# Optimization experiments

Hardware: AMD Instinct MI355X
Metric: run time of the kernel (lower is better)

Reference implementation:

```python
import jax, jax.numpy as jnp
import numpy as np

D_MODEL = 1024
N_HEADS = 16
D_K = D_MODEL // N_HEADS
B, T = 2, 2048


def setup_inputs() -> dict:
    key = jax.random.key(0)
    ks = jax.random.split(key, 9)
    s = 1.0 / np.sqrt(D_MODEL)
    def lin(kw, kb):
        W = jax.random.uniform(kw, (D_MODEL, D_MODEL), jnp.float32, -s, s)
        b = jax.random.uniform(kb, (D_MODEL,), jnp.float32, -s, s)
        return W, b
    Wq, bq = lin(ks[0], ks[1])
    Wk, bk = lin(ks[2], ks[3])
    Wv, bv = lin(ks[4], ks[5])
    Wo, bo = lin(ks[6], ks[7])
    x = jax.random.normal(ks[8], (B, T, D_MODEL), jnp.float32)
    return {"x": x, "Wq": Wq, "bq": bq, "Wk": Wk, "bk": bk,
            "Wv": Wv, "bv": bv, "Wo": Wo, "bo": bo}


def reference(x, Wq, bq, Wk, bk, Wv, bv, Wo, bo):
    Bn, Tn, _ = x.shape
    # torch Linear: x @ W.T + b
    def proj(W, b):
        y = x @ W.T + b  # [B, T, D]
        return y.reshape(Bn, Tn, N_HEADS, D_K).transpose(0, 2, 1, 3)  # [B, H, T, d_k]
    q = proj(Wq, bq)
    k = proj(Wk, bk)
    v = proj(Wv, bv)
    scores = jnp.einsum('bhqd,bhkd->bhqk', q, k) / jnp.sqrt(jnp.float32(D_K))
    causal = jnp.tril(jnp.ones((Tn, Tn), dtype=bool))  # True = keep
    scores = jnp.where(causal[None, None], scores, -jnp.inf)
    attn = jax.nn.softmax(scores, axis=-1)
    # dropout is identity in eval mode
    ctx = jnp.einsum('bhqk,bhkd->bhqd', attn, v)
    ctx = ctx.transpose(0, 2, 1, 3).reshape(Bn, Tn, D_MODEL)
    return ctx @ Wo.T + bo
```

## Files before the change

### kernel.cpp

```cpp
#include <hip/hip_runtime.h>
#include <hip/hip_bf16.h>
#include <stdint.h>

#define D_MODEL 1024
#define NH 16
#define DK 64
#define BB 2
#define TT 2048
#define NROWS (BB*TT)

#define QSCALE 0.180336880f

typedef short bf16x8 __attribute__((ext_vector_type(8)));
typedef short bf16x4 __attribute__((ext_vector_type(4)));
typedef float f32x4  __attribute__((ext_vector_type(4)));

#if __has_builtin(__builtin_amdgcn_mfma_f32_16x16x16_bf16)
  #define MFMA16(a,b,c) __builtin_amdgcn_mfma_f32_16x16x16_bf16(a,b,c,0,0,0)
  #define HAVE_M16 1
#elif __has_builtin(__builtin_amdgcn_mfma_f32_16x16x16bf16_1k)
  #define MFMA16(a,b,c) __builtin_amdgcn_mfma_f32_16x16x16bf16_1k(a,b,c,0,0,0)
  #define HAVE_M16 1
#else
  #define HAVE_M16 0
#endif

#if __has_builtin(__builtin_amdgcn_global_load_lds)
  #define HAVE_GLDS 1
__device__ __forceinline__ void gload16(const unsigned short* g, unsigned short* lds){
    __builtin_amdgcn_global_load_lds(
        (const __attribute__((address_space(1))) unsigned int*)g,
        (__attribute__((address_space(3))) unsigned int*)lds, 16, 0, 0);
}
#else
  #define HAVE_GLDS 0
#endif

__device__ __forceinline__ float fexp2(float x){
#if __has_builtin(__builtin_amdgcn_exp2f)
    return __builtin_amdgcn_exp2f(x);
#else
    return exp2f(x);
#endif
}

__device__ __forceinline__ unsigned pkbf(float a, float b){
    float2 t; t.x = a; t.y = b;
    __hip_bfloat162 h = __float22bfloat162_rn(t);
    return *reinterpret_cast<unsigned*>(&h);
}
__device__ __forceinline__ unsigned short bfbits(float a){
    __hip_bfloat16 h = __float2bfloat16(a);
    return *reinterpret_cast<unsigned short*>(&h);
}

__global__ __launch_bounds__(256) void conv_all(
    const float* __restrict__ x,
    const float* __restrict__ Wq, const float* __restrict__ Wk,
    const float* __restrict__ Wv, const float* __restrict__ Wo,
    unsigned short* __restrict__ xb, unsigned short* __restrict__ wb)
{
    const int blk = blockIdx.x;
    const float* src; unsigned short* dst; size_t i;
    if (blk < 2048) {
        src = x; dst = xb;
        i = ((size_t)blk * 256 + threadIdx.x) * 8;
    } else {
        const int t = (blk - 2048) >> 9;
        src = (t == 0) ? Wq : (t == 1) ? Wk : (t == 2) ? Wv : Wo;
        dst = wb + (size_t)t * D_MODEL * D_MODEL;
        i = ((size_t)((blk - 2048) & 511) * 256 + threadIdx.x) * 8;
    }
    float4 a = *(const float4*)(src + i);
    float4 b = *(const float4*)(src + i + 4);
    uint4 w;
    w.x = pkbf(a.x, a.y); w.y = pkbf(a.z, a.w);
    w.z = pkbf(b.x, b.y); w.w = pkbf(b.z, b.w);
    *(uint4*)(dst + i) = w;
}

__global__ __launch_bounds__(256) void conv_bf16(
    const float* __restrict__ x, unsigned short* __restrict__ y)
{
    size_t i = ((size_t)blockIdx.x * 256 + threadIdx.x) * 8;
    float4 a = *(const float4*)(x + i);
    float4 b = *(const float4*)(x + i + 4);
    uint4 w;
    w.x = pkbf(a.x, a.y); w.y = pkbf(a.z, a.w);
    w.z = pkbf(b.x, b.y); w.w = pkbf(b.z, b.w);
    *(uint4*)(y + i) = w;
}

#if HAVE_GLDS
template<int MI, int NB, bool CF32>
__device__ __forceinline__ void gemm_async(
    const unsigned short* __restrict__ Ap, const unsigned short* __restrict__ Bp,
    const float* __restrict__ bias, void* __restrict__ Cp,
    bool vt, float scale, unsigned short* As, unsigned short* Bs)
{
    constexpr int BMt = MI * 32, BNt = NB * 32;
    const int K = D_MODEL, N = D_MODEL;
    const int tid  = threadIdx.x;
    const int m0   = blockIdx.y * BMt;
    const int n0   = blockIdx.x * BNt;
    const int lane = tid & 63;
    const int w    = tid >> 6;
    const int wm   = (w >> 1) * (MI * 16);
    const int wn   = (w &  1) * (BNt / 2);
    const int l16  = lane & 15;
    const int quad = lane >> 4;
    const int crow = lane >> 2;
    const int ccol = (lane & 3) * 8;

    constexpr int CA = MI / 2;
    constexpr int CB = NB / 2;

    auto issue = [&](int buf, int k0){
        #pragma unroll
        for (int c = 0; c < CA; ++c) {
            const int chunk = w * CA + c;
            gload16(Ap + (size_t)(m0 + chunk*16 + crow) * K + k0 + ccol,
                    As + buf * BMt * 32 + chunk * 512);
        }
        #pragma unroll
        for (int c = 0; c < CB; ++c) {
            const int chunk = w * CB + c;
            gload16(Bp + (size_t)(n0 + chunk*16 + crow) * K + k0 + ccol,
                    Bs + buf * BNt * 32 + chunk * 512);
        }
    };

    f32x4 acc[MI][NB] = {};
    issue(0, 0);

    constexpr int ITER = D_MODEL / 32;
    for (int it = 0; it < ITER; ++it) {
        __syncthreads();
        if (it + 1 < ITER) issue((it + 1) & 1, (it + 1) * 32);
        const unsigned short* A = As + (it & 1) * BMt * 32;
        const unsigned short* B = Bs + (it & 1) * BNt * 32;
        bf16x8 af[MI], bg[NB];
        #pragma unroll
        for (int i = 0; i < MI; ++i)
            af[i] = *(const bf16x8*)&A[(wm + 16*i + l16) * 32 + quad * 8];
        #pragma unroll
        for (int j = 0; j < NB; ++j)
            bg[j] = *(const bf16x8*)&B[(wn + 16*j + l16) * 32 + quad * 8];
        #pragma unroll
        for (int i = 0; i < MI; ++i)
            #pragma unroll
            for (int j = 0; j < NB; ++j)
                acc[i][j] = __builtin_amdgcn_mfma_f32_16x16x32_bf16(af[i], bg[j], acc[i][j], 0, 0, 0);
    }

    #pragma unroll
    for (int j = 0; j < NB; ++j) {
        const int n = n0 + wn + 16*j + l16;
        const float bj = bias[n];
        #pragma unroll
        for (int i = 0; i < MI; ++i) {
            const int m = m0 + wm + 16*i + quad*4;
            if (vt) {
                const int b = m >> 11, t = m & 2047;
                ushort4 wv;
                wv.x = bfbits(acc[i][j][0] + bj);
                wv.y = bfbits(acc[i][j][1] + bj);
                wv.z = bfbits(acc[i][j][2] + bj);
                wv.w = bfbits(acc[i][j][3] + bj);
                *(ushort4*)((unsigned short*)Cp + (size_t)b * D_MODEL * TT
                            + (size_t)n * TT + t) = wv;
            } else {
                #pragma unroll
                for (int r = 0; r < 4; ++r) {
                    float v = (acc[i][j][r] + bj) * scale;
                    if (CF32) ((float*)Cp)[(size_t)(m + r) * N + n] = v;
                    else      ((__hip_bfloat16*)Cp)[(size_t)(m + r) * N + n] = __float2bfloat16(v);
                }
            }
        }
    }
}
#endif

#define ASTR 40

template<int MI, int NB, bool AF32, bool BF32, bool CF32>
__device__ __forceinline__ void gemm_body(
    const void* __restrict__ Ap, const void* __restrict__ Bp,
    const float* __restrict__ bias, void* __restrict__ Cp,
    bool vt, float scale, unsigned short* As, unsigned short* Bs)
{
    constexpr int BMt = MI * 32, BNt = NB * 32;
    const int K = D_MODEL, N = D_MODEL;
    const int tid  = threadIdx.x;
    const int m0   = blockIdx.y * BMt;
    const int n0   = blockIdx.x * BNt;
    const int lane = tid & 63;
    const int wave = tid >> 6;
    const int wm   = (wave >> 1) * (MI * 16);
    const int wn   = (wave &  1) * (BNt / 2);
    const int l16  = lane & 15;
    const int quad = lane >> 4;
    const int ar = (MI == 4) ? (tid >> 1) : (tid >> 2);
    const int ac = (MI == 4) ? ((tid & 1) * 16) : ((tid & 3) * 8);
    const int br = (NB == 4) ? (tid >> 1) : (tid >> 2);
    const int bc = (NB == 4) ? ((tid & 1) * 16) : ((tid & 3) * 8);

    uint4 pa[4], pb[4];

    auto loadA = [&](int k0){
        if (AF32) {
            const float* p = (const float*)Ap + (size_t)(m0 + ar) * K + k0 + ac;
            pa[0] = *(const uint4*)(p);     pa[1] = *(const uint4*)(p + 4);
            if (MI == 4) { pa[2] = *(const uint4*)(p + 8); pa[3] = *(const uint4*)(p + 12); }
        } else {
            const unsigned short* p = (const unsigned short*)Ap + (size_t)(m0 + ar) * K + k0 + ac;
            pa[0] = *(const uint4*)(p);
            if (MI == 4) pa[1] = *(const uint4*)(p + 8);
        }
    };
    auto loadB = [&](int k0){
        if (BF32) {
            const float* p = (const float*)Bp + (size_t)(n0 + br) * K + k0 + bc;
            pb[0] = *(const uint4*)(p); pb[1] = *(const uint4*)(p + 4);
            if (NB == 4) { pb[2] = *(const uint4*)(p + 8); pb[3] = *(const uint4*)(p + 12); }
        } else {
            const unsigned short* p = (const unsigned short*)Bp + (size_t)(n0 + br) * K + k0 + bc;
            pb[0] = *(const uint4*)(p);
            if (NB == 4) pb[1] = *(const uint4*)(p + 8);
        }
    };
    auto stage = [&](int buf){
        unsigned short* A = As + buf * BMt * ASTR;
        unsigned short* B = Bs + buf * BNt * ASTR;
        if (AF32) {
            const float* f = (const float*)pa;
            uint4 w0;
            w0.x = pkbf(f[0], f[1]); w0.y = pkbf(f[2], f[3]);
            w0.z = pkbf(f[4], f[5]); w0.w = pkbf(f[6], f[7]);
            *(uint4*)&A[ar*ASTR + ac] = w0;
            if (MI == 4) {
                uint4 w1;
                w1.x = pkbf(f[8], f[9]);   w1.y = pkbf(f[10], f[11]);
                w1.z = pkbf(f[12], f[13]); w1.w = pkbf(f[14], f[15]);
                *(uint4*)&A[ar*ASTR + ac + 8] = w1;
            }
        } else {
            *(uint4*)&A[ar*ASTR + ac] = pa[0];
            if (MI == 4) *(uint4*)&A[ar*ASTR + ac + 8] = pa[1];
        }
        if (BF32) {
            const float* g = (const float*)pb;
            uint4 v0;
            v0.x = pkbf(g[0], g[1]); v0.y = pkbf(g[2], g[3]);
            v0.z = pkbf(g[4], g[5]); v0.w = pkbf(g[6], g[7]);
            *(uint4*)&B[br*ASTR + bc] = v0;
            if (NB == 4) {
                uint4 v1;
                v1.x = pkbf(g[8], g[9]);   v1.y = pkbf(g[10], g[11]);
                v1.z = pkbf(g[12], g[13]); v1.w = pkbf(g[14], g[15]);
                *(uint4*)&B[br*ASTR + bc + 8] = v1;
            }
        } else {
            *(uint4*)&B[br*ASTR + bc] = pb[0];
            if (NB == 4) *(uint4*)&B[br*ASTR + bc + 8] = pb[1];
        }
    };

    f32x4 acc[MI][NB] = {};
    loadA(0); loadB(0);
    stage(0);

    constexpr int ITER = D_MODEL / 32;
    for (int it = 0; it < ITER; ++it) {
        __syncthreads();
        if (it + 1 < ITER) { loadA((it + 1) * 32); loadB((it + 1) * 32); }
        const unsigned short* A = As + (it & 1) * BMt * ASTR;
        const unsigned short* B = Bs + (it & 1) * BNt * ASTR;
        bf16x8 af[MI], bg[NB];
        #pragma unroll
        for (int i = 0; i < MI; ++i)
            af[i] = *(const bf16x8*)&A[(wm + 16*i + l16) * ASTR + quad * 8];
        #pragma unroll
        for (int j = 0; j < NB; ++j)
            bg[j] = *(const bf16x8*)&B[(wn + 16*j + l16) * ASTR + quad * 8];
        #pragma unroll
        for (int i = 0; i < MI; ++i)
            #pragma unroll
            for (int j = 0; j < NB; ++j)
                acc[i][j] = __builtin_amdgcn_mfma_f32_16x16x32_bf16(af[i], bg[j], acc[i][j], 0, 0, 0);
        if (it + 1 < ITER) stage((it + 1) & 1);
    }

    #pragma unroll
    for (int j = 0; j < NB; ++j) {
        const int n = n0 + wn + 16*j + l16;
        const float bj = bias[n];
        #pragma unroll
        for (int i = 0; i < MI; ++i) {
            const int m = m0 + wm + 16*i + quad*4;
            if (vt) {
                const int b = m >> 11, t = m & 2047;
                ushort4 wv;
                wv.x = bfbits(acc[i][j][0] + bj);
                wv.y = bfbits(acc[i][j][1] + bj);
                wv.z = bfbits(acc[i][j][2] + bj);
                wv.w = bfbits(acc[i][j][3] + bj);
                *(ushort4*)((unsigned short*)Cp + (size_t)b * D_MODEL * TT
                            + (size_t)n * TT + t) = wv;
            } else {
                #pragma unroll
                for (int r = 0; r < 4; ++r) {
                    float v = (acc[i][j][r] + bj) * scale;
                    if (CF32) ((float*)Cp)[(size_t)(m + r) * N + n] = v;
                    else      ((__hip_bfloat16*)Cp)[(size_t)(m + r) * N + n] = __float2bfloat16(v);
                }
            }
        }
    }
}

template<bool AF32, bool BF32>
__device__ __forceinline__ void qkv_sel(
    const void* x,
    const void* Wq, const float* bq, const void* Wk, const float* bk,
    const void* Wv, const float* bv,
    __hip_bfloat16* Qw, __hip_bfloat16* Kd, __hip_bfloat16* Vd,
    unsigned short* As, unsigned short* Bs)
{
    const void* W; const float* bi; void* C; bool vt = false; float sc = 1.0f;
    if      (blockIdx.z == 0) { W = Wq; bi = bq; C = Qw; sc = QSCALE; }
    else if (blockIdx.z == 1) { W = Wk; bi = bk; C = Kd; }
    else                      { W = Wv; bi = bv; C = Vd; vt = true; }
    gemm_body<4, 4, AF32, BF32, false>(x, W, bi, C, vt, sc, As, Bs);
}

#define QKV_KERNEL(name, AF, BF, XT)                                          \
__global__ __launch_bounds__(256, 3) void name(                               \
    const XT* __restrict__ x,                                                 \
    const void* __restrict__ Wq, const float* __restrict__ bq,                \
    const void* __restrict__ Wk, const float* __restrict__ bk,                \
    const void* __restrict__ Wv, const float* __restrict__ bv,                \
    __hip_bfloat16* __restrict__ Qw, __hip_bfloat16* __restrict__ Kd,         \
    __hip_bfloat16* __restrict__ Vd)                                          \
{                                                                             \
    __shared__ __align__(16) unsigned short As[2*128*ASTR];                   \
    __shared__ __align__(16) unsigned short Bs[2*128*ASTR];                   \
    qkv_sel<AF, BF>(x, Wq, bq, Wk, bk, Wv, bv, Qw, Kd, Vd, As, Bs);           \
}
QKV_KERNEL(gemm_qkv_f32, true,  true,  float)
QKV_KERNEL(gemm_qkv_xb,  false, true,  unsigned short)

__global__ __launch_bounds__(256, 3) void gemm_qkv_bb(
    const unsigned short* __restrict__ x,
    const unsigned short* __restrict__ Wq, const float* __restrict__ bq,
    const unsigned short* __restrict__ Wk, const float* __restrict__ bk,
    const unsigned short* __restrict__ Wv, const float* __restrict__ bv,
    __hip_bfloat16* __restrict__ Qw, __hip_bfloat16* __restrict__ Kd,
    __hip_bfloat16* __restrict__ Vd)
{
#if HAVE_GLDS
    __shared__ __align__(16) unsigned short As[2*128*32];
    __shared__ __align__(16) unsigned short Bs[2*128*32];
    const unsigned short* W; const float* bi; void* C; bool vt = false; float sc = 1.0f;
    if      (blockIdx.z == 0) { W = Wq; bi = bq; C = Qw; sc = QSCALE; }
    else if (blockIdx.z == 1) { W = Wk; bi = bk; C = Kd; }
    else                      { W = Wv; bi = bv; C = Vd; vt = true; }
    gemm_async<4, 4, false>(x, W, bi, C, vt, sc, As, Bs);
#else
    __shared__ __align__(16) unsigned short As[2*128*ASTR];
    __shared__ __align__(16) unsigned short Bs[2*128*ASTR];
    qkv_sel<false, false>(x, Wq, bq, Wk, bk, Wv, bv, Qw, Kd, Vd, As, Bs);
#endif
}

__global__ __launch_bounds__(256, 2) void gemm_out_f(
    const __hip_bfloat16* __restrict__ ctx, const void* __restrict__ Wo,
    const float* __restrict__ bo, float* __restrict__ out)
{
    __shared__ __align__(16) unsigned short As[2*128*ASTR];
    __shared__ __align__(16) unsigned short Bs[2*64*ASTR];
    gemm_body<4, 2, false, true, true>(ctx, Wo, bo, out, false, 1.0f, As, Bs);
}

__global__ __launch_bounds__(256, 2) void gemm_out_b(
    const __hip_bfloat16* __restrict__ ctx, const unsigned short* __restrict__ Wo,
    const float* __restrict__ bo, float* __restrict__ out)
{
#if HAVE_GLDS
    __shared__ __align__(16) unsigned short As[2*128*32];
    __shared__ __align__(16) unsigned short Bs[2*64*32];
    gemm_async<4, 2, true>((const unsigned short*)ctx, Wo, bo, out, false, 1.0f, As, Bs);
#else
    __shared__ __align__(16) unsigned short As[2*128*ASTR];
    __shared__ __align__(16) unsigned short Bs[2*64*ASTR];
    gemm_body<4, 2, false, false, true>(ctx, Wo, bo, out, false, 1.0f, As, Bs);
#endif
}

#define QSTR 68

__global__ __launch_bounds__(256, 2) void attn_mfma(
    const __hip_bfloat16* __restrict__ Q,
    const __hip_bfloat16* __restrict__ Km,
    const __hip_bfloat16* __restrict__ Vt,
    __hip_bfloat16* __restrict__ ctx)
{
    __shared__ __align__(16) unsigned short Ks [2][64*QSTR];
    __shared__ __align__(16) unsigned short VTs[2][64*QSTR];
#if !HAVE_M16
    __shared__ __align__(16) unsigned short QP[64*QSTR];
#endif

    const int tid = threadIdx.x;
    const int blk = blockIdx.x;
    const int i4 = blk & 255;
    const int j4 = blk >> 8;
    const int ql = (j4 & 1) ? 15 - (i4 & 15) : (i4 & 15);
    const int qh = 31 - ql;
    const int bh = (i4 >> 4) + (j4 << 4);
    const int b  = bh >> 4;
    const int h  = bh & 15;
    const int q0l = ql << 6;
    const int q0h = qh << 6;
    const size_t rowbase = (size_t)b * TT;
    const int colbase = h * DK;

    const int lane = tid & 63;
    const int w    = tid >> 6;
    const int l16  = lane & 15;
    const int quad = lane >> 4;
    const int lr = tid >> 2;
    const int lc = (tid & 3) << 4;

    const unsigned short* Vtb = (const unsigned short*)Vt + (size_t)b * D_MODEL * TT;

    uint4 kr0, kr1, vt0, vt1;
    auto prefetch = [&](int kv0){
        const unsigned short* pk = (const unsigned short*)Km +
            (rowbase + kv0 + lr) * D_MODEL + colbase + lc;
        kr0 = *(const uint4*)(pk);
        kr1 = *(const uint4*)(pk + 8);
        const unsigned short* pv = Vtb + (size_t)(colbase + lr) * TT + kv0 + lc;
        vt0 = *(const uint4*)(pv);
        vt1 = *(const uint4*)(pv + 8);
    };
    auto stageKV = [&](int buf){
        *(uint4*)&Ks [buf][lr*QSTR + lc]     = kr0;
        *(uint4*)&Ks [buf][lr*QSTR + lc + 8] = kr1;
        *(uint4*)&VTs[buf][lr*QSTR + lc]     = vt0;
        *(uint4*)&VTs[buf][lr*QSTR + lc + 8] = vt1;
    };

#if HAVE_M16
    const unsigned short* qpl = (const unsigned short*)Q +
        (rowbase + q0l + 16*w + l16) * D_MODEL + colbase + quad*8;
    bf16x8 af_ql0 = *(const bf16x8*)(qpl);
    bf16x8 af_ql1 = *(const bf16x8*)(qpl + 32);
    const unsigned short* qph = (const unsigned short*)Q +
        (rowbase + q0h + 16*w + l16) * D_MODEL + colbase + quad*8;
    bf16x8 af_qh0 = *(const bf16x8*)(qph);
    bf16x8 af_qh1 = *(const bf16x8*)(qph + 32);

    prefetch(0);
    stageKV(0);

    f32x4 ol[4] = {}, oh[4] = {};
    float lpl = 0.0f, lph = 0.0f;

    auto softmax_t = [&](f32x4* s, bf16x4* bp, float& lp, bool diag){
        #pragma unroll
        for (int cb = 0; cb < 4; ++cb) {
            float p[4];
            #pragma unroll
            for (int r = 0; r < 4; ++r) {
                float v = fminf(s[cb][r], 36.0f);
                bool keep = !diag || (16*cb + quad*4 + r <= 16*w + l16);
                p[r] = keep ? fexp2(v) : 0.0f;
                lp += p[r];
            }
            uint2 u; u.x = pkbf(p[0], p[1]); u.y = pkbf(p[2], p[3]);
            bp[cb] = *reinterpret_cast<bf16x4*>(&u);
        }
    };

    for (int kt = 0; kt <= ql; ++kt) {
        __syncthreads();
        prefetch((kt + 1) << 6);
        const int cur = kt & 1;

        f32x4 sl[4] = {}, sh[4] = {};
        #pragma unroll
        for (int cb = 0; cb < 4; ++cb) {
            bf16x8 ak0 = *(const bf16x8*)&Ks[cur][(16*cb + l16)*QSTR + quad*8];
            bf16x8 ak1 = *(const bf16x8*)&Ks[cur][(16*cb + l16)*QSTR + quad*8 + 32];
            sl[cb] = __builtin_amdgcn_mfma_f32_16x16x32_bf16(ak0, af_ql0, sl[cb], 0, 0, 0);
            sl[cb] = __builtin_amdgcn_mfma_f32_16x16x32_bf16(ak1, af_ql1, sl[cb], 0, 0, 0);
            sh[cb] = __builtin_amdgcn_mfma_f32_16x16x32_bf16(ak0, af_qh0, sh[cb], 0, 0, 0);
            sh[cb] = __builtin_amdgcn_mfma_f32_16x16x32_bf16(ak1, af_qh1, sh[cb], 0, 0, 0);
        }

        bf16x4 bpl[4], bph[4];
        if (kt == ql) softmax_t(sl, bpl, lpl, true);
        else          softmax_t(sl, bpl, lpl, false);
        softmax_t(sh, bph, lph, false);

        #pragma unroll
        for (int nb = 0; nb < 4; ++nb)
            #pragma unroll
            for (int cb = 0; cb < 4; ++cb) {
                bf16x4 av = *(const bf16x4*)&VTs[cur][(16*nb + l16)*QSTR + 16*cb + quad*4];
                ol[nb] = MFMA16(av, bpl[cb], ol[nb]);
                oh[nb] = MFMA16(av, bph[cb], oh[nb]);
            }

        stageKV((kt + 1) & 1);
    }

    for (int kt = ql + 1; kt <= qh; ++kt) {
        __syncthreads();
        if (kt < qh) prefetch((kt + 1) << 6);
        const int cur = kt & 1;

        f32x4 sh[4] = {};
        #pragma unroll
        for (int cb = 0; cb < 4; ++cb) {
            bf16x8 ak0 = *(const bf16x8*)&Ks[cur][(16*cb + l16)*QSTR + quad*8];
            bf16x8 ak1 = *(const bf16x8*)&Ks[cur][(16*cb + l16)*QSTR + quad*8 + 32];
            sh[cb] = __builtin_amdgcn_mfma_f32_16x16x32_bf16(ak0, af_qh0, sh[cb], 0, 0, 0);
            sh[cb] = __builtin_amdgcn_mfma_f32_16x16x32_bf16(ak1, af_qh1, sh[cb], 0, 0, 0);
        }

        bf16x4 bph[4];
        if (kt == qh) softmax_t(sh, bph, lph, true);
        else          softmax_t(sh, bph, lph, false);

        #pragma unroll
        for (int nb = 0; nb < 4; ++nb)
            #pragma unroll
            for (int cb = 0; cb < 4; ++cb) {
                bf16x4 av = *(const bf16x4*)&VTs[cur][(16*nb + l16)*QSTR + 16*cb + quad*4];
                oh[nb] = MFMA16(av, bph[cb], oh[nb]);
            }

        if (kt < qh) stageKV((kt + 1) & 1);
    }

    auto finish = [&](f32x4* o, float lp, int q0t){
        lp += __shfl_xor(lp, 16);
        lp += __shfl_xor(lp, 32);
        const float inv_l = 1.0f / lp;
        const size_t row = (rowbase + q0t + 16*w + l16) * (size_t)D_MODEL + colbase;
        #pragma unroll
        for (int nb = 0; nb < 4; ++nb) {
            ushort4 wv;
            wv.x = bfbits(o[nb][0] * inv_l);
            wv.y = bfbits(o[nb][1] * inv_l);
            wv.z = bfbits(o[nb][2] * inv_l);
            wv.w = bfbits(o[nb][3] * inv_l);
            *(ushort4*)((unsigned short*)ctx + row + 16*nb + quad*4) = wv;
        }
    };
    finish(ol, lpl, q0l);
    finish(oh, lph, q0h);
#else
    const short ob = (short)0x3F80;
    bf16x8 ones = { ob, ob, ob, ob, ob, ob, ob, ob };

    for (int sel = 0; sel < 2; ++sel) {
        const int qt = sel ? qh : ql;
        const int q0 = qt << 6;

        __syncthreads();
        {
            const unsigned short* p = (const unsigned short*)Q +
                (rowbase + q0 + lr) * D_MODEL + colbase + lc;
            *(uint4*)&QP[lr*QSTR + lc]     = *(const uint4*)(p);
            *(uint4*)&QP[lr*QSTR + lc + 8] = *(const uint4*)(p + 8);
        }
        prefetch(0);
        __syncthreads();
        bf16x8 af_q0 = *(const bf16x8*)&QP[(16*w + l16)*QSTR + quad*8];
        bf16x8 af_q1 = *(const bf16x8*)&QP[(16*w + l16)*QSTR + quad*8 + 32];
        stageKV(0);

        f32x4 o[4] = {};
        f32x4 l_acc = {};

        for (int kt = 0; kt <= qt; ++kt) {
            __syncthreads();
            if (kt < qt) prefetch((kt + 1) << 6);
            const int cur = kt & 1;

            f32x4 s[4] = {};
            #pragma unroll
            for (int cb = 0; cb < 4; ++cb) {
                bf16x8 bk0 = *(const bf16x8*)&Ks[cur][(16*cb + l16)*QSTR + quad*8];
                bf16x8 bk1 = *(const bf16x8*)&Ks[cur][(16*cb + l16)*QSTR + quad*8 + 32];
                s[cb] = __builtin_amdgcn_mfma_f32_16x16x32_bf16(af_q0, bk0, s[cb], 0, 0, 0);
                s[cb] = __builtin_amdgcn_mfma_f32_16x16x32_bf16(af_q1, bk1, s[cb], 0, 0, 0);
            }
            const bool diag = (kt == qt);
            #pragma unroll
            for (int cb = 0; cb < 4; ++cb)
                #pragma unroll
                for (int r = 0; r < 4; ++r) {
                    float v = fminf(s[cb][r], 36.0f);
                    float p = (diag && (16*cb + l16 > 16*w + quad*4 + r)) ? 0.0f : fexp2(v);
                    QP[(16*w + quad*4 + r)*QSTR + 16*cb + l16] = bfbits(p);
                }
            bf16x8 ap0 = *(const bf16x8*)&QP[(16*w + l16)*QSTR + quad*8];
            bf16x8 ap1 = *(const bf16x8*)&QP[(16*w + l16)*QSTR + quad*8 + 32];
            #pragma unroll
            for (int nb = 0; nb < 4; ++nb) {
                bf16x8 bv0 = *(const bf16x8*)&VTs[cur][(16*nb + l16)*QSTR + quad*8];
                bf16x8 bv1 = *(const bf16x8*)&VTs[cur][(16*nb + l16)*QSTR + quad*8 + 32];
                o[nb] = __builtin_amdgcn_mfma_f32_16x16x32_bf16(ap0, bv0, o[nb], 0, 0, 0);
                o[nb] = __builtin_amdgcn_mfma_f32_16x16x32_bf16(ap1, bv1, o[nb], 0, 0, 0);
            }
            l_acc = __builtin_amdgcn_mfma_f32_16x16x32_bf16(ap0, ones, l_acc, 0, 0, 0);
            l_acc = __builtin_amdgcn_mfma_f32_16x16x32_bf16(ap1, ones, l_acc, 0, 0, 0);
            if (kt < qt) stageKV((kt + 1) & 1);
        }
        float inv_l[4];
        #pragma unroll
        for (int r = 0; r < 4; ++r) inv_l[r] = 1.0f / l_acc[r];
        #pragma unroll
        for (int nb = 0; nb < 4; ++nb)
            #pragma unroll
            for (int r = 0; r < 4; ++r) {
                const int row = q0 + 16*w + quad*4 + r;
                ctx[(rowbase + row)*D_MODEL + colbase + 16*nb + l16] =
                    __float2bfloat16(o[nb][r] * inv_l[r]);
            }
    }
#endif
}

extern "C" void kernel_launch(void* const* d_in, const int* in_sizes, int n_in,
                              void* d_out, int out_size, void* d_ws, size_t ws_size,
                              hipStream_t stream) {
    const float* x  = (const float*)d_in[0];
    const float* Wq = (const float*)d_in[1];
    const float* bq = (const float*)d_in[2];
    const float* Wk = (const float*)d_in[3];
    const float* bk = (const float*)d_in[4];
    const float* Wv = (const float*)d_in[5];
    const float* bv = (const float*)d_in[6];
    const float* Wo = (const float*)d_in[7];
    const float* bo = (const float*)d_in[8];

    __hip_bfloat16* Qw = (__hip_bfloat16*)d_ws;
    __hip_bfloat16* Kd = (__hip_bfloat16*)d_out;
    __hip_bfloat16* Vd = Kd + (size_t)NROWS * D_MODEL;
    unsigned short* xb = (unsigned short*)d_ws + (size_t)NROWS * D_MODEL;
    unsigned short* wb = xb + (size_t)NROWS * D_MODEL;
    const size_t WSZ = (size_t)D_MODEL * D_MODEL;

    dim3 gqkv(D_MODEL / 128, NROWS / 128, 3);
    dim3 gout(D_MODEL / 64, NROWS / 128);
    const bool haveXB = ws_size >= (size_t)(16u << 20);
    const bool haveWB = ws_size >= (size_t)(24u << 20);

    if (haveWB) {
        conv_all<<<4096, 256, 0, stream>>>(x, Wq, Wk, Wv, Wo, xb, wb);
        gemm_qkv_bb<<<gqkv, 256, 0, stream>>>(xb, wb, bq, wb + WSZ, bk,
                                              wb + 2*WSZ, bv, Qw, Kd, Vd);
    } else if (haveXB) {
        conv_bf16<<<(NROWS * D_MODEL) / (256 * 8), 256, 0, stream>>>(x, xb);
        gemm_qkv_xb<<<gqkv, 256, 0, stream>>>(xb, Wq, bq, Wk, bk, Wv, bv, Qw, Kd, Vd);
    } else {
        gemm_qkv_f32<<<gqkv, 256, 0, stream>>>(x, Wq, bq, Wk, bk, Wv, bv, Qw, Kd, Vd);
    }

    attn_mfma<<<BB * NH * (TT / 128), 256, 0, stream>>>(Qw, Kd, Vd, Qw);

    if (haveWB)
        gemm_out_b<<<gout, 256, 0, stream>>>(Qw, wb + 3*WSZ, bo, (float*)d_out);
    else
        gemm_out_f<<<gout, 256, 0, stream>>>(Qw, Wo, bo, (float*)d_out);
}
```

Before: 182.5 us.

## Unroll out-proj K loop, remap attention blocks per XCD, MFMA row sums, setprio

The output-projection GEMM now stages two 32-wide K slices per barrier, which halves the number of syncs at the cost of twice the LDS. The attention kernel remaps block indices so that the blocks for each batch-head group land on the same XCD, aiming for better L2 reuse of K and V. Softmax row sums are now accumulated with an MFMA against a ones vector instead of scalar adds plus cross-lane shuffles. MFMA sections are also wrapped in s_setprio to favour matrix issue across waves.

```diff
diff --git a/kernel.cpp b/kernel.cpp
--- a/kernel.cpp
+++ b/kernel.cpp
@@ -92,7 +92,7 @@
 }
 
 #if HAVE_GLDS
-template<int MI, int NB, bool CF32>
+template<int MI, int NB, bool CF32, int KU>
 __device__ __forceinline__ void gemm_async(
     const unsigned short* __restrict__ Ap, const unsigned short* __restrict__ Bp,
     const float* __restrict__ bias, void* __restrict__ Cp,
@@ -115,42 +115,48 @@
     constexpr int CA = MI / 2;
     constexpr int CB = NB / 2;
 
-    auto issue = [&](int buf, int k0){
-        #pragma unroll
-        for (int c = 0; c < CA; ++c) {
-            const int chunk = w * CA + c;
-            gload16(Ap + (size_t)(m0 + chunk*16 + crow) * K + k0 + ccol,
-                    As + buf * BMt * 32 + chunk * 512);
-        }
-        #pragma unroll
-        for (int c = 0; c < CB; ++c) {
-            const int chunk = w * CB + c;
-            gload16(Bp + (size_t)(n0 + chunk*16 + crow) * K + k0 + ccol,
-                    Bs + buf * BNt * 32 + chunk * 512);
+    auto issue = [&](int grp, int k0){
+        #pragma unroll
+        for (int u = 0; u < KU; ++u) {
+            #pragma unroll
+            for (int c = 0; c < CA; ++c) {
+                const int chunk = w * CA + c;
+                gload16(Ap + (size_t)(m0 + chunk*16 + crow) * K + k0 + u*32 + ccol,
+                        As + (grp*KU + u) * BMt * 32 + chunk * 512);
+            }
+            #pragma unroll
+            for (int c = 0; c < CB; ++c) {
+                const int chunk = w * CB + c;
+                gload16(Bp + (size_t)(n0 + chunk*16 + crow) * K + k0 + u*32 + ccol,
+                        Bs + (grp*KU + u) * BNt * 32 + chunk * 512);
+            }
         }
     };
 
     f32x4 acc[MI][NB] = {};
     issue(0, 0);
 
-    constexpr int ITER = D_MODEL / 32;
-    for (int it = 0; it < ITER; ++it) {
+    constexpr int NG = D_MODEL / (32 * KU);
+    for (int g = 0; g < NG; ++g) {
         __syncthreads();
-        if (it + 1 < ITER) issue((it + 1) & 1, (it + 1) * 32);
-        const unsigned short* A = As + (it & 1) * BMt * 32;
-        const unsigned short* B = Bs + (it & 1) * BNt * 32;
-        bf16x8 af[MI], bg[NB];
-        #pragma unroll
-        for (int i = 0; i < MI; ++i)
-            af[i] = *(const bf16x8*)&A[(wm + 16*i + l16) * 32 + quad * 8];
-        #pragma unroll
-        for (int j = 0; j < NB; ++j)
-            bg[j] = *(const bf16x8*)&B[(wn + 16*j + l16) * 32 + quad * 8];
-        #pragma unroll
-        for (int i = 0; i < MI; ++i)
+        if (g + 1 < NG) issue((g + 1) & 1, (g + 1) * (32 * KU));
+        #pragma unroll
+        for (int u = 0; u < KU; ++u) {
+            const unsigned short* A = As + ((g & 1) * KU + u) * BMt * 32;
+            const unsigned short* B = Bs + ((g & 1) * KU + u) * BNt * 32;
+            bf16x8 af[MI], bg[NB];
+            #pragma unroll
+            for (int i = 0; i < MI; ++i)
+                af[i] = *(const bf16x8*)&A[(wm + 16*i + l16) * 32 + quad * 8];
             #pragma unroll
             for (int j = 0; j < NB; ++j)
-                acc[i][j] = __builtin_amdgcn_mfma_f32_16x16x32_bf16(af[i], bg[j], acc[i][j], 0, 0, 0);
+                bg[j] = *(const bf16x8*)&B[(wn + 16*j + l16) * 32 + quad * 8];
+            #pragma unroll
+            for (int i = 0; i < MI; ++i)
+                #pragma unroll
+                for (int j = 0; j < NB; ++j)
+                    acc[i][j] = __builtin_amdgcn_mfma_f32_16x16x32_bf16(af[i], bg[j], acc[i][j], 0, 0, 0);
+        }
     }
 
     #pragma unroll
@@ -366,7 +372,7 @@
     if      (blockIdx.z == 0) { W = Wq; bi = bq; C = Qw; sc = QSCALE; }
     else if (blockIdx.z == 1) { W = Wk; bi = bk; C = Kd; }
     else                      { W = Wv; bi = bv; C = Vd; vt = true; }
-    gemm_async<4, 4, false>(x, W, bi, C, vt, sc, As, Bs);
+    gemm_async<4, 4, false, 1>(x, W, bi, C, vt, sc, As, Bs);
 #else
     __shared__ __align__(16) unsigned short As[2*128*ASTR];
     __shared__ __align__(16) unsigned short Bs[2*128*ASTR];
@@ -388,9 +394,9 @@
     const float* __restrict__ bo, float* __restrict__ out)
 {
 #if HAVE_GLDS
-    __shared__ __align__(16) unsigned short As[2*128*32];
-    __shared__ __align__(16) unsigned short Bs[2*64*32];
-    gemm_async<4, 2, true>((const unsigned short*)ctx, Wo, bo, out, false, 1.0f, As, Bs);
+    __shared__ __align__(16) unsigned short As[2*2*128*32];
+    __shared__ __align__(16) unsigned short Bs[2*2*64*32];
+    gemm_async<4, 2, true, 2>((const unsigned short*)ctx, Wo, bo, out, false, 1.0f, As, Bs);
 #else
     __shared__ __align__(16) unsigned short As[2*128*ASTR];
     __shared__ __align__(16) unsigned short Bs[2*64*ASTR];
@@ -414,13 +420,14 @@
 
     const int tid = threadIdx.x;
     const int blk = blockIdx.x;
-    const int i4 = blk & 255;
-    const int j4 = blk >> 8;
-    const int ql = (j4 & 1) ? 15 - (i4 & 15) : (i4 & 15);
-    const int qh = 31 - ql;
-    const int bh = (i4 >> 4) + (j4 << 4);
-    const int b  = bh >> 4;
-    const int h  = bh & 15;
+    const int xcd = blk & 7;
+    const int s   = blk >> 3;
+    const int bh  = xcd * 4 + (s & 3);
+    const int qi  = s >> 2;
+    const int ql  = (qi < 8) ? qi : 23 - qi;
+    const int qh  = 31 - ql;
+    const int b   = bh >> 4;
+    const int h   = bh & 15;
     const int q0l = ql << 6;
     const int q0h = qh << 6;
     const size_t rowbase = (size_t)b * TT;
@@ -466,18 +473,19 @@
     stageKV(0);
 
     f32x4 ol[4] = {}, oh[4] = {};
-    float lpl = 0.0f, lph = 0.0f;
-
-    auto softmax_t = [&](f32x4* s, bf16x4* bp, float& lp, bool diag){
+    f32x4 lsl = {}, lsh = {};
+    const short ob = (short)0x3F80;
+    const bf16x4 ones4 = { ob, ob, ob, ob };
+
+    auto softmax_t = [&](f32x4* sarr, bf16x4* bp, bool diag){
         #pragma unroll
         for (int cb = 0; cb < 4; ++cb) {
             float p[4];
             #pragma unroll
             for (int r = 0; r < 4; ++r) {
-                float v = fminf(s[cb][r], 36.0f);
+                float v = fminf(sarr[cb][r], 36.0f);
                 bool keep = !diag || (16*cb + quad*4 + r <= 16*w + l16);
                 p[r] = keep ? fexp2(v) : 0.0f;
-                lp += p[r];
             }
             uint2 u; u.x = pkbf(p[0], p[1]); u.y = pkbf(p[2], p[3]);
             bp[cb] = *reinterpret_cast<bf16x4*>(&u);
@@ -490,6 +498,7 @@
         const int cur = kt & 1;
 
         f32x4 sl[4] = {}, sh[4] = {};
+        __builtin_amdgcn_s_setprio(1);
         #pragma unroll
         for (int cb = 0; cb < 4; ++cb) {
             bf16x8 ak0 = *(const bf16x8*)&Ks[cur][(16*cb + l16)*QSTR + quad*8];
@@ -499,12 +508,19 @@
             sh[cb] = __builtin_amdgcn_mfma_f32_16x16x32_bf16(ak0, af_qh0, sh[cb], 0, 0, 0);
             sh[cb] = __builtin_amdgcn_mfma_f32_16x16x32_bf16(ak1, af_qh1, sh[cb], 0, 0, 0);
         }
+        __builtin_amdgcn_s_setprio(0);
 
         bf16x4 bpl[4], bph[4];
-        if (kt == ql) softmax_t(sl, bpl, lpl, true);
-        else          softmax_t(sl, bpl, lpl, false);
-        softmax_t(sh, bph, lph, false);
-
+        if (kt == ql) softmax_t(sl, bpl, true);
+        else          softmax_t(sl, bpl, false);
+        softmax_t(sh, bph, false);
+
+        __builtin_amdgcn_s_setprio(1);
+        #pragma unroll
+        for (int cb = 0; cb < 4; ++cb) {
+            lsl = MFMA16(ones4, bpl[cb], lsl);
+            lsh = MFMA16(ones4, bph[cb], lsh);
+        }
         #pragma unroll
         for (int nb = 0; nb < 4; ++nb)
             #pragma unroll
@@ -513,6 +529,7 @@
                 ol[nb] = MFMA16(av, bpl[cb], ol[nb]);
                 oh[nb] = MFMA16(av, bph[cb], oh[nb]);
             }
+        __builtin_amdgcn_s_setprio(0);
 
         stageKV((kt + 1) & 1);
     }
@@ -523,6 +540,7 @@
         const int cur = kt & 1;
 
         f32x4 sh[4] = {};
+        __builtin_amdgcn_s_setprio(1);
         #pragma unroll
         for (int cb = 0; cb < 4; ++cb) {
             bf16x8 ak0 = *(const bf16x8*)&Ks[cur][(16*cb + l16)*QSTR + quad*8];
@@ -530,11 +548,16 @@
             sh[cb] = __builtin_amdgcn_mfma_f32_16x16x32_bf16(ak0, af_qh0, sh[cb], 0, 0, 0);
             sh[cb] = __builtin_amdgcn_mfma_f32_16x16x32_bf16(ak1, af_qh1, sh[cb], 0, 0, 0);
         }
+        __builtin_amdgcn_s_setprio(0);
 
         bf16x4 bph[4];
-        if (kt == qh) softmax_t(sh, bph, lph, true);
-        else          softmax_t(sh, bph, lph, false);
-
+        if (kt == qh) softmax_t(sh, bph, true);
+        else          softmax_t(sh, bph, false);
+
+        __builtin_amdgcn_s_setprio(1);
+        #pragma unroll
+        for (int cb = 0; cb < 4; ++cb)
+            lsh = MFMA16(ones4, bph[cb], lsh);
         #pragma unroll
         for (int nb = 0; nb < 4; ++nb)
             #pragma unroll
@@ -542,13 +565,12 @@
                 bf16x4 av = *(const bf16x4*)&VTs[cur][(16*nb + l16)*QSTR + 16*cb + quad*4];
                 oh[nb] = MFMA16(av, bph[cb], oh[nb]);
             }
+        __builtin_amdgcn_s_setprio(0);
 
         if (kt < qh) stageKV((kt + 1) & 1);
     }
 
     auto finish = [&](f32x4* o, float lp, int q0t){
-        lp += __shfl_xor(lp, 16);
-        lp += __shfl_xor(lp, 32);
         const float inv_l = 1.0f / lp;
         const size_t row = (rowbase + q0t + 16*w + l16) * (size_t)D_MODEL + colbase;
         #pragma unroll
@@ -561,8 +583,8 @@
             *(ushort4*)((unsigned short*)ctx + row + 16*nb + quad*4) = wv;
         }
     };
-    finish(ol, lpl, q0l);
-    finish(oh, lph, q0h);
+    finish(ol, lsl[0], q0l);
+    finish(oh, lsh[0], q0h);
 #else
     const short ob = (short)0x3F80;
     bf16x8 ones = { ob, ob, ob, ob, ob, ob, ob, ob };
```

New measurement: 182.3 us. Within noise of the previous version (-0.1%).
